# Kernel tuning notes

Hardware: AMD Instinct MI355X
Metric: run time of the kernel (lower is better)

The kernel has to match this reference:

```python
import jax, jax.numpy as jnp
import numpy as np

B, H, S, D, R = 2, 32, 1024, 128, 16
NB = 4  # max blocks: pre-image, image, pre-assistant-end, post-assistant


def _make_block_mask():
    # Synthetic but realistic block boundaries per sample (derived from the
    # image-token run and assistant-token subsequence positions that the torch
    # module extracts host-side from input_ids).
    bounds = [
        [(0, 16), (16, 272), (272, 603), (603, S)],
        [(0, 8), (8, 264), (264, 501), (501, S)],
    ]
    m = np.zeros((B, NB, S), np.float32)
    for b, blocks in enumerate(bounds):
        for n, (s, e) in enumerate(blocks):
            m[b, n, s:e] = 1.0
    return jnp.asarray(m)


def setup_inputs() -> dict:
    key = jax.random.key(0)
    ks = jax.random.split(key, 7)
    hid = H * D  # 4096
    lo = H * R   # 512
    causal_masked = ~jnp.tril(jnp.ones((S, S), bool))  # True = masked
    return {
        "query_states": jax.random.normal(ks[0], (B, H, S, D), jnp.float32),
        "key_states": jax.random.normal(ks[1], (B, H, S, D), jnp.float32),
        "Wqa": jax.random.normal(ks[2], (lo, hid), jnp.float32) / np.sqrt(hid),
        "Wqb": jax.random.normal(ks[3], (hid, lo), jnp.float32) / np.sqrt(lo),
        "Wka": jax.random.normal(ks[4], (lo, hid), jnp.float32) / np.sqrt(hid),
        "Wkb": jax.random.normal(ks[5], (hid, lo), jnp.float32) / np.sqrt(lo),
        "alpha": jax.random.normal(ks[6], (1,), jnp.float32) * 0.01,  # alpha_std
        "block_mask": _make_block_mask(),  # [B, NB, K] 1.0 inside block
        "attention_mask": jnp.broadcast_to(causal_masked, (B, 1, S, S)),
    }


def reference(query_states, key_states, Wqa, Wqb, Wka, Wkb, alpha, block_mask, attention_mask):
    Bb, Hh, Q, Dd = query_states.shape
    scaling = Dd ** -0.5

    # low-rank Q projection: [B,H,Q,D] -> [B,Q,H*D] -> rank -> back
    q = query_states.transpose(0, 2, 1, 3).reshape(Bb, Q, Hh * Dd)
    q = (q @ Wqa.T) @ Wqb.T
    q = q.reshape(Bb, Q, Hh, Dd).transpose(0, 2, 1, 3)

    Kk = key_states.shape[2]
    k = key_states.transpose(0, 2, 1, 3).reshape(Bb, Kk, Hh * Dd)
    k = (k @ Wka.T) @ Wkb.T
    k = k.reshape(Bb, Kk, Hh, Dd).transpose(0, 2, 1, 3)

    scores = jnp.einsum('bhqd,bhkd->bhqk', q, k) * scaling  # [B,H,Q,K]
    neg = jnp.finfo(scores.dtype).min
    scores = jnp.where(attention_mask, neg, scores)
    attn = jax.nn.softmax(scores, axis=-1)

    # block-wise mean pooling with causal-valid counts (mean_pool path)
    valid = (~attention_mask[:, 0]).astype(attn.dtype)       # [B,Q,K]
    masked_attn = attn * valid[:, None]                      # zero masked keys
    counts = jnp.einsum('bqk,bnk->bqn', valid, block_mask)   # [B,Q,NB]
    sums = jnp.einsum('bhqk,bnk->bhqn', masked_attn, block_mask)
    block_scores = sums / jnp.maximum(counts, 1.0)[:, None]  # [B,H,Q,NB]

    # expand block scores back to full [B,H,Q,K] and zero masked positions
    reweight = jnp.einsum('bhqn,bnk->bhqk', block_scores, block_mask)
    reweight = reweight * valid[:, None]
    return alpha[0] * reweight
```

## Files before the change

kernel.cpp:

```cpp
#include <hip/hip_runtime.h>
#include <hip/hip_bf16.h>

typedef float  f32x4 __attribute__((ext_vector_type(4)));
typedef _Float16 f16x8 __attribute__((ext_vector_type(8)));

#define S_LEN 1024
#define NHEAD 32
#define DHEAD 128
#define HID   4096
#define LORA  512
#define MROWS 2048

__global__ __launch_bounds__(256) void proj1_kernel(
    const float* __restrict__ Xq, const float* __restrict__ Wq_,
    const float* __restrict__ Xk, const float* __restrict__ Wk_,
    _Float16* __restrict__ Uq, _Float16* __restrict__ Uk)
{
  const float* X = blockIdx.z ? Xk : Xq;
  const float* W = blockIdx.z ? Wk_ : Wq_;
  _Float16*    U = blockIdx.z ? Uk  : Uq;

  __shared__ _Float16 As[128 * 40];
  __shared__ _Float16 Bs[64 * 40];

  const int t = threadIdx.x;
  const int lane = t & 63, w = t >> 6;
  const int wr = w >> 1, wc = w & 1;
  const int m0 = blockIdx.x * 128, n0 = blockIdx.y * 64;

  const int ar = t >> 1, ac = (t & 1) * 16;
  const int am = m0 + ar, ab = am >> 10, as_ = am & 1023;
  const float* Abase = X + (size_t)ab * (NHEAD * S_LEN * DHEAD) + (size_t)as_ * DHEAD;
  const int br = t >> 2, bc = (t & 3) * 8;
  const float* Brow = W + (size_t)(n0 + br) * HID;

  f32x4 acc[4][2] = {};

  for (int kt = 0; kt < HID / 32; ++kt) {
    const int kg = kt * 32 + ac;
    const float* pa = Abase + (size_t)(kg >> 7) * (S_LEN * DHEAD) + (kg & 127);
    f32x4 v0 = *(const f32x4*)(pa + 0);
    f32x4 v1 = *(const f32x4*)(pa + 4);
    f32x4 v2 = *(const f32x4*)(pa + 8);
    f32x4 v3 = *(const f32x4*)(pa + 12);
    f16x8 h0, h1;
#pragma unroll
    for (int i = 0; i < 4; ++i) {
      h0[i] = (_Float16)v0[i]; h0[i + 4] = (_Float16)v1[i];
      h1[i] = (_Float16)v2[i]; h1[i + 4] = (_Float16)v3[i];
    }
    const float* pb = Brow + kt * 32 + bc;
    f32x4 u0 = *(const f32x4*)(pb + 0);
    f32x4 u1 = *(const f32x4*)(pb + 4);
    f16x8 hb;
#pragma unroll
    for (int i = 0; i < 4; ++i) { hb[i] = (_Float16)u0[i]; hb[i + 4] = (_Float16)u1[i]; }

    __syncthreads();
    *(f16x8*)&As[ar * 40 + ac]     = h0;
    *(f16x8*)&As[ar * 40 + ac + 8] = h1;
    *(f16x8*)&Bs[br * 40 + bc]     = hb;
    __syncthreads();

    f16x8 afr[4], bfr[2];
#pragma unroll
    for (int im = 0; im < 4; ++im)
      afr[im] = *(const f16x8*)&As[(wr * 64 + im * 16 + (lane & 15)) * 40 + (lane >> 4) * 8];
#pragma unroll
    for (int in = 0; in < 2; ++in)
      bfr[in] = *(const f16x8*)&Bs[(wc * 32 + in * 16 + (lane & 15)) * 40 + (lane >> 4) * 8];
#pragma unroll
    for (int im = 0; im < 4; ++im)
#pragma unroll
      for (int in = 0; in < 2; ++in)
        acc[im][in] = __builtin_amdgcn_mfma_f32_16x16x32_f16(afr[im], bfr[in], acc[im][in], 0, 0, 0);
  }

#pragma unroll
  for (int im = 0; im < 4; ++im)
#pragma unroll
    for (int in = 0; in < 2; ++in)
#pragma unroll
      for (int j = 0; j < 4; ++j) {
        const int m = m0 + wr * 64 + im * 16 + (lane >> 4) * 4 + j;
        const int n = n0 + wc * 32 + in * 16 + (lane & 15);
        U[(size_t)m * LORA + n] = (_Float16)acc[im][in][j];
      }
}

__global__ __launch_bounds__(256) void proj2_kernel(
    const _Float16* __restrict__ Uq, const float* __restrict__ Wq_,
    const _Float16* __restrict__ Uk, const float* __restrict__ Wk_,
    _Float16* __restrict__ Pq, _Float16* __restrict__ Pk)
{
  const _Float16* U = blockIdx.z ? Uk : Uq;
  const float*    W = blockIdx.z ? Wk_ : Wq_;
  _Float16*       P = blockIdx.z ? Pk : Pq;

  __shared__ _Float16 As[128 * 40];
  __shared__ _Float16 Bs[64 * 40];

  const int t = threadIdx.x;
  const int lane = t & 63, w = t >> 6;
  const int wr = w >> 1, wc = w & 1;
  const int m0 = blockIdx.x * 128, n0 = blockIdx.y * 64;

  const int ar = t >> 1, ac = (t & 1) * 16;
  const _Float16* Arow = U + (size_t)(m0 + ar) * LORA;
  const int br = t >> 2, bc = (t & 3) * 8;
  const float* Brow = W + (size_t)(n0 + br) * LORA;

  f32x4 acc[4][2] = {};

  for (int kt = 0; kt < LORA / 32; ++kt) {
    const _Float16* pa = Arow + kt * 32 + ac;
    f16x8 h0 = *(const f16x8*)(pa + 0);
    f16x8 h1 = *(const f16x8*)(pa + 8);
    const float* pb = Brow + kt * 32 + bc;
    f32x4 u0 = *(const f32x4*)(pb + 0);
    f32x4 u1 = *(const f32x4*)(pb + 4);
    f16x8 hb;
#pragma unroll
    for (int i = 0; i < 4; ++i) { hb[i] = (_Float16)u0[i]; hb[i + 4] = (_Float16)u1[i]; }

    __syncthreads();
    *(f16x8*)&As[ar * 40 + ac]     = h0;
    *(f16x8*)&As[ar * 40 + ac + 8] = h1;
    *(f16x8*)&Bs[br * 40 + bc]     = hb;
    __syncthreads();

    f16x8 afr[4], bfr[2];
#pragma unroll
    for (int im = 0; im < 4; ++im)
      afr[im] = *(const f16x8*)&As[(wr * 64 + im * 16 + (lane & 15)) * 40 + (lane >> 4) * 8];
#pragma unroll
    for (int in = 0; in < 2; ++in)
      bfr[in] = *(const f16x8*)&Bs[(wc * 32 + in * 16 + (lane & 15)) * 40 + (lane >> 4) * 8];
#pragma unroll
    for (int im = 0; im < 4; ++im)
#pragma unroll
      for (int in = 0; in < 2; ++in)
        acc[im][in] = __builtin_amdgcn_mfma_f32_16x16x32_f16(afr[im], bfr[in], acc[im][in], 0, 0, 0);
  }

#pragma unroll
  for (int im = 0; im < 4; ++im)
#pragma unroll
    for (int in = 0; in < 2; ++in)
#pragma unroll
      for (int j = 0; j < 4; ++j) {
        const int m = m0 + wr * 64 + im * 16 + (lane >> 4) * 4 + j;
        const int n = n0 + wc * 32 + in * 16 + (lane & 15);
        P[(size_t)m * HID + n] = (_Float16)acc[im][in][j];
      }
}

__global__ __launch_bounds__(256) void attn_kernel(
    const _Float16* __restrict__ QP, const _Float16* __restrict__ KP,
    const float* __restrict__ bmask, const float* __restrict__ alphap,
    float* __restrict__ out)
{
  __shared__ float    bm[1024 * 4];
  __shared__ _Float16 kv[64 * 136];
  __shared__ float    bs_l[64 * 4];

  const int t = threadIdx.x;
  const int lane = t & 63, w = t >> 6;
  const int bh = blockIdx.x, b = bh >> 5, h = bh & 31;
  const int qb = (int)(gridDim.y - 1) - (int)blockIdx.y;

  for (int idx = t; idx < 4096; idx += 256) {
    const int nb = idx >> 10, k = idx & 1023;
    bm[k * 4 + nb] = bmask[(size_t)b * 4096 + idx];
  }

  const int qrow = qb * 64 + w * 16 + (lane & 15);
  const _Float16* qrp = QP + (size_t)(b * 1024 + qrow) * HID + h * DHEAD;
  f16x8 a[4];
#pragma unroll
  for (int i = 0; i < 4; ++i)
    a[i] = *(const f16x8*)(qrp + i * 32 + (lane >> 4) * 8);

  float L[4] = {0.f, 0.f, 0.f, 0.f};
  float bsum[4][4] = {};
  float cnt[4][4] = {};
  const float scale = 0.08838834764831845f;

  const int r = t >> 2, c = (t & 3) * 32;
  const _Float16* kbase = KP + (size_t)(b * 1024) * HID + h * DHEAD;

  for (int kt = 0; kt <= qb; ++kt) {
    const _Float16* pk = kbase + (size_t)(kt * 64 + r) * HID + c;
    f16x8 k0 = *(const f16x8*)(pk + 0);
    f16x8 k1 = *(const f16x8*)(pk + 8);
    f16x8 k2 = *(const f16x8*)(pk + 16);
    f16x8 k3 = *(const f16x8*)(pk + 24);
    __syncthreads();
    *(f16x8*)&kv[r * 136 + c + 0]  = k0;
    *(f16x8*)&kv[r * 136 + c + 8]  = k1;
    *(f16x8*)&kv[r * 136 + c + 16] = k2;
    *(f16x8*)&kv[r * 136 + c + 24] = k3;
    __syncthreads();

#pragma unroll
    for (int nt = 0; nt < 4; ++nt) {
      f32x4 sacc = {0.f, 0.f, 0.f, 0.f};
#pragma unroll
      for (int i = 0; i < 4; ++i) {
        f16x8 bf = *(const f16x8*)&kv[(nt * 16 + (lane & 15)) * 136 + i * 32 + (lane >> 4) * 8];
        sacc = __builtin_amdgcn_mfma_f32_16x16x32_f16(a[i], bf, sacc, 0, 0, 0);
      }
      const int kk = kt * 64 + nt * 16 + (lane & 15);
      f32x4 mv = *(const f32x4*)&bm[kk * 4];
#pragma unroll
      for (int j = 0; j < 4; ++j) {
        const int q = qb * 64 + w * 16 + (lane >> 4) * 4 + j;
        const bool valid = (kk <= q);
        const float e = valid ? __expf(sacc[j] * scale) : 0.f;
        const float vf = valid ? 1.f : 0.f;
        L[j] += e;
        bsum[0][j] += e * mv[0];  cnt[0][j] += vf * mv[0];
        bsum[1][j] += e * mv[1];  cnt[1][j] += vf * mv[1];
        bsum[2][j] += e * mv[2];  cnt[2][j] += vf * mv[2];
        bsum[3][j] += e * mv[3];  cnt[3][j] += vf * mv[3];
      }
    }
  }

#pragma unroll
  for (int j = 0; j < 4; ++j) {
#pragma unroll
    for (int m = 1; m < 16; m <<= 1) {
      L[j] += __shfl_xor(L[j], m, 64);
#pragma unroll
      for (int nb = 0; nb < 4; ++nb) {
        bsum[nb][j] += __shfl_xor(bsum[nb][j], m, 64);
        cnt[nb][j]  += __shfl_xor(cnt[nb][j], m, 64);
      }
    }
  }
  if ((lane & 15) == 0) {
#pragma unroll
    for (int j = 0; j < 4; ++j) {
      const int rr = w * 16 + (lane >> 4) * 4 + j;
      const float invL = 1.f / L[j];
#pragma unroll
      for (int nb = 0; nb < 4; ++nb)
        bs_l[rr * 4 + nb] = bsum[nb][j] * invL / fmaxf(cnt[nb][j], 1.f);
    }
  }
  __syncthreads();

  const float alpha = alphap[0];
  const size_t obase = ((size_t)bh * 1024 + (size_t)qb * 64) * 1024;
  for (int rr = 0; rr < 64; ++rr) {
    const int q = qb * 64 + rr;
    f32x4 bsv = *(const f32x4*)&bs_l[rr * 4];
    const int k0 = t * 4;
    f32x4 m0v = *(const f32x4*)&bm[(k0 + 0) * 4];
    f32x4 m1v = *(const f32x4*)&bm[(k0 + 1) * 4];
    f32x4 m2v = *(const f32x4*)&bm[(k0 + 2) * 4];
    f32x4 m3v = *(const f32x4*)&bm[(k0 + 3) * 4];
    f32x4 o;
    o[0] = (k0 + 0 <= q) ? alpha * (bsv[0]*m0v[0] + bsv[1]*m0v[1] + bsv[2]*m0v[2] + bsv[3]*m0v[3]) : 0.f;
    o[1] = (k0 + 1 <= q) ? alpha * (bsv[0]*m1v[0] + bsv[1]*m1v[1] + bsv[2]*m1v[2] + bsv[3]*m1v[3]) : 0.f;
    o[2] = (k0 + 2 <= q) ? alpha * (bsv[0]*m2v[0] + bsv[1]*m2v[1] + bsv[2]*m2v[2] + bsv[3]*m2v[3]) : 0.f;
    o[3] = (k0 + 3 <= q) ? alpha * (bsv[0]*m3v[0] + bsv[1]*m3v[1] + bsv[2]*m3v[2] + bsv[3]*m3v[3]) : 0.f;
    *(f32x4*)(out + obase + (size_t)rr * 1024 + k0) = o;
  }
}

extern "C" void kernel_launch(void* const* d_in, const int* in_sizes, int n_in,
                              void* d_out, int out_size, void* d_ws, size_t ws_size,
                              hipStream_t stream) {
  const float* q     = (const float*)d_in[0];
  const float* k     = (const float*)d_in[1];
  const float* Wqa   = (const float*)d_in[2];
  const float* Wqb   = (const float*)d_in[3];
  const float* Wka   = (const float*)d_in[4];
  const float* Wkb   = (const float*)d_in[5];
  const float* alpha = (const float*)d_in[6];
  const float* bmask = (const float*)d_in[7];
  float* out = (float*)d_out;

  _Float16* Uq = (_Float16*)d_ws;
  _Float16* Uk = Uq + (size_t)MROWS * LORA;
  _Float16* Pq = Uk + (size_t)MROWS * LORA;
  _Float16* Pk = Pq + (size_t)MROWS * HID;

  proj1_kernel<<<dim3(16, 8, 2),  256, 0, stream>>>(q, Wqa, k, Wka, Uq, Uk);
  proj2_kernel<<<dim3(16, 64, 2), 256, 0, stream>>>(Uq, Wqb, Uk, Wkb, Pq, Pk);
  attn_kernel <<<dim3(64, 16),    256, 0, stream>>>(Pq, Pk, bmask, alpha, out);
}
```

Measured before the change: 538.4 us.

## Pre-convert inputs to fp16, use LDS-direct GEMM, simplify attention block sums

Adds a conversion kernel that casts activations (into token-major layout) and weights to fp16 up front. The two projections are replaced by one shared GEMM that loads tiles straight into LDS with global_load_lds on 128x128 tiles, dropping the per-tile conversion in the main loop. The attention kernel now takes causal counts from a prefix sum of the block mask, gets the softmax denominator from the block sums, and skips fully masked MFMA tiles on the diagonal. This adds a full extra pass over memory for conversion and leaves only 128 blocks for the first GEMM. The LDS tiles are unpadded, so bank conflicts may increase.

```diff
diff --git a/kernel.cpp b/kernel.cpp
--- a/kernel.cpp
+++ b/kernel.cpp
@@ -1,8 +1,9 @@
 #include <hip/hip_runtime.h>
 #include <hip/hip_bf16.h>
 
-typedef float  f32x4 __attribute__((ext_vector_type(4)));
+typedef float    f32x4 __attribute__((ext_vector_type(4)));
 typedef _Float16 f16x8 __attribute__((ext_vector_type(8)));
+typedef unsigned int u32;
 
 #define S_LEN 1024
 #define NHEAD 32
@@ -11,147 +12,113 @@
 #define LORA  512
 #define MROWS 2048
 
-__global__ __launch_bounds__(256) void proj1_kernel(
-    const float* __restrict__ Xq, const float* __restrict__ Wq_,
-    const float* __restrict__ Xk, const float* __restrict__ Wk_,
-    _Float16* __restrict__ Uq, _Float16* __restrict__ Uk)
+__device__ __forceinline__ void gload16(const void* g, const void* l) {
+  __builtin_amdgcn_global_load_lds(
+      (const __attribute__((address_space(1))) u32*)g,
+      (__attribute__((address_space(3))) u32*)l, 16, 0, 0);
+}
+
+#define XCH  1048576
+#define WCH  262144
+#define TOTCH (2*XCH + 4*WCH)
+
+__global__ __launch_bounds__(256) void convert_kernel(
+    const float* __restrict__ Xq, const float* __restrict__ Xk,
+    const float* __restrict__ Wqa, const float* __restrict__ Wka,
+    const float* __restrict__ Wqb, const float* __restrict__ Wkb,
+    _Float16* __restrict__ XqH, _Float16* __restrict__ XkH,
+    _Float16* __restrict__ WaqH, _Float16* __restrict__ WakH,
+    _Float16* __restrict__ WbqH, _Float16* __restrict__ WbkH)
 {
-  const float* X = blockIdx.z ? Xk : Xq;
-  const float* W = blockIdx.z ? Wk_ : Wq_;
-  _Float16*    U = blockIdx.z ? Uk  : Uq;
-
-  __shared__ _Float16 As[128 * 40];
-  __shared__ _Float16 Bs[64 * 40];
-
-  const int t = threadIdx.x;
-  const int lane = t & 63, w = t >> 6;
+  for (int c = blockIdx.x * 256 + threadIdx.x; c < TOTCH; c += 2048 * 256) {
+    const float* src;
+    _Float16* dst;
+    if (c < 2 * XCH) {
+      const int cc = (c < XCH) ? c : c - XCH;
+      const float* X = (c < XCH) ? Xq : Xk;
+      _Float16*  XH = (c < XCH) ? XqH : XkH;
+      const int row = cc >> 9;
+      const int col8 = cc & 511;
+      const int h = col8 >> 4, d0 = (col8 & 15) * 8;
+      const int b = row >> 10, s = row & 1023;
+      src = X + (((size_t)(b * NHEAD + h)) * S_LEN + s) * DHEAD + d0;
+      dst = XH + (size_t)row * HID + col8 * 8;
+    } else {
+      const int cw = c - 2 * XCH;
+      const int seg = cw / WCH;
+      const int off = (cw - seg * WCH) * 8;
+      const float* Ws[4] = {Wqa, Wka, Wqb, Wkb};
+      _Float16*  Wd[4] = {WaqH, WakH, WbqH, WbkH};
+      src = Ws[seg] + off;
+      dst = Wd[seg] + off;
+    }
+    f32x4 v0 = *(const f32x4*)(src + 0);
+    f32x4 v1 = *(const f32x4*)(src + 4);
+    f16x8 h8;
+#pragma unroll
+    for (int i = 0; i < 4; ++i) { h8[i] = (_Float16)v0[i]; h8[i + 4] = (_Float16)v1[i]; }
+    *(f16x8*)dst = h8;
+  }
+}
+
+__global__ __launch_bounds__(256) void gemm_f16(
+    const _Float16* __restrict__ Aq, const _Float16* __restrict__ Bq,
+    _Float16* __restrict__ Cq,
+    const _Float16* __restrict__ Ak, const _Float16* __restrict__ Bk,
+    _Float16* __restrict__ Ck, int K, int N)
+{
+  const _Float16* A = blockIdx.z ? Ak : Aq;
+  const _Float16* B = blockIdx.z ? Bk : Bq;
+  _Float16*       C = blockIdx.z ? Ck : Cq;
+
+  __shared__ _Float16 As[128 * 32];
+  __shared__ _Float16 Bs[128 * 32];
+
+  const int t = threadIdx.x, lane = t & 63, w = t >> 6;
   const int wr = w >> 1, wc = w & 1;
-  const int m0 = blockIdx.x * 128, n0 = blockIdx.y * 64;
-
-  const int ar = t >> 1, ac = (t & 1) * 16;
-  const int am = m0 + ar, ab = am >> 10, as_ = am & 1023;
-  const float* Abase = X + (size_t)ab * (NHEAD * S_LEN * DHEAD) + (size_t)as_ * DHEAD;
-  const int br = t >> 2, bc = (t & 3) * 8;
-  const float* Brow = W + (size_t)(n0 + br) * HID;
-
-  f32x4 acc[4][2] = {};
-
-  for (int kt = 0; kt < HID / 32; ++kt) {
-    const int kg = kt * 32 + ac;
-    const float* pa = Abase + (size_t)(kg >> 7) * (S_LEN * DHEAD) + (kg & 127);
-    f32x4 v0 = *(const f32x4*)(pa + 0);
-    f32x4 v1 = *(const f32x4*)(pa + 4);
-    f32x4 v2 = *(const f32x4*)(pa + 8);
-    f32x4 v3 = *(const f32x4*)(pa + 12);
-    f16x8 h0, h1;
-#pragma unroll
-    for (int i = 0; i < 4; ++i) {
-      h0[i] = (_Float16)v0[i]; h0[i + 4] = (_Float16)v1[i];
-      h1[i] = (_Float16)v2[i]; h1[i + 4] = (_Float16)v3[i];
-    }
-    const float* pb = Brow + kt * 32 + bc;
-    f32x4 u0 = *(const f32x4*)(pb + 0);
-    f32x4 u1 = *(const f32x4*)(pb + 4);
-    f16x8 hb;
-#pragma unroll
-    for (int i = 0; i < 4; ++i) { hb[i] = (_Float16)u0[i]; hb[i + 4] = (_Float16)u1[i]; }
-
-    __syncthreads();
-    *(f16x8*)&As[ar * 40 + ac]     = h0;
-    *(f16x8*)&As[ar * 40 + ac + 8] = h1;
-    *(f16x8*)&Bs[br * 40 + bc]     = hb;
-    __syncthreads();
-
-    f16x8 afr[4], bfr[2];
+  const int m0 = blockIdx.x * 128, n0 = blockIdx.y * 128;
+
+  const int o0 = w * 1024 + lane * 16;
+  const int o1 = o0 + 4096;
+  const int r0 = o0 >> 6, k0e = (o0 & 63) >> 1;
+  const int r1 = o1 >> 6, k1e = (o1 & 63) >> 1;
+
+  char* AsB = (char*)As;
+  char* BsB = (char*)Bs;
+
+  f32x4 acc[4][4] = {};
+
+  for (int kt = 0; kt < K; kt += 32) {
+    __syncthreads();
+    gload16(A + (size_t)(m0 + r0) * K + kt + k0e, AsB + w * 1024);
+    gload16(A + (size_t)(m0 + r1) * K + kt + k1e, AsB + 4096 + w * 1024);
+    gload16(B + (size_t)(n0 + r0) * K + kt + k0e, BsB + w * 1024);
+    gload16(B + (size_t)(n0 + r1) * K + kt + k1e, BsB + 4096 + w * 1024);
+    __syncthreads();
+
+    f16x8 af[4], bf[4];
 #pragma unroll
     for (int im = 0; im < 4; ++im)
-      afr[im] = *(const f16x8*)&As[(wr * 64 + im * 16 + (lane & 15)) * 40 + (lane >> 4) * 8];
-#pragma unroll
-    for (int in = 0; in < 2; ++in)
-      bfr[in] = *(const f16x8*)&Bs[(wc * 32 + in * 16 + (lane & 15)) * 40 + (lane >> 4) * 8];
+      af[im] = *(const f16x8*)(AsB + (wr * 64 + im * 16 + (lane & 15)) * 64 + (lane >> 4) * 16);
+#pragma unroll
+    for (int in = 0; in < 4; ++in)
+      bf[in] = *(const f16x8*)(BsB + (wc * 64 + in * 16 + (lane & 15)) * 64 + (lane >> 4) * 16);
 #pragma unroll
     for (int im = 0; im < 4; ++im)
 #pragma unroll
-      for (int in = 0; in < 2; ++in)
-        acc[im][in] = __builtin_amdgcn_mfma_f32_16x16x32_f16(afr[im], bfr[in], acc[im][in], 0, 0, 0);
+      for (int in = 0; in < 4; ++in)
+        acc[im][in] = __builtin_amdgcn_mfma_f32_16x16x32_f16(af[im], bf[in], acc[im][in], 0, 0, 0);
   }
 
 #pragma unroll
   for (int im = 0; im < 4; ++im)
 #pragma unroll
-    for (int in = 0; in < 2; ++in)
+    for (int in = 0; in < 4; ++in)
 #pragma unroll
       for (int j = 0; j < 4; ++j) {
         const int m = m0 + wr * 64 + im * 16 + (lane >> 4) * 4 + j;
-        const int n = n0 + wc * 32 + in * 16 + (lane & 15);
-        U[(size_t)m * LORA + n] = (_Float16)acc[im][in][j];
-      }
-}
-
-__global__ __launch_bounds__(256) void proj2_kernel(
-    const _Float16* __restrict__ Uq, const float* __restrict__ Wq_,
-    const _Float16* __restrict__ Uk, const float* __restrict__ Wk_,
-    _Float16* __restrict__ Pq, _Float16* __restrict__ Pk)
-{
-  const _Float16* U = blockIdx.z ? Uk : Uq;
-  const float*    W = blockIdx.z ? Wk_ : Wq_;
-  _Float16*       P = blockIdx.z ? Pk : Pq;
-
-  __shared__ _Float16 As[128 * 40];
-  __shared__ _Float16 Bs[64 * 40];
-
-  const int t = threadIdx.x;
-  const int lane = t & 63, w = t >> 6;
-  const int wr = w >> 1, wc = w & 1;
-  const int m0 = blockIdx.x * 128, n0 = blockIdx.y * 64;
-
-  const int ar = t >> 1, ac = (t & 1) * 16;
-  const _Float16* Arow = U + (size_t)(m0 + ar) * LORA;
-  const int br = t >> 2, bc = (t & 3) * 8;
-  const float* Brow = W + (size_t)(n0 + br) * LORA;
-
-  f32x4 acc[4][2] = {};
-
-  for (int kt = 0; kt < LORA / 32; ++kt) {
-    const _Float16* pa = Arow + kt * 32 + ac;
-    f16x8 h0 = *(const f16x8*)(pa + 0);
-    f16x8 h1 = *(const f16x8*)(pa + 8);
-    const float* pb = Brow + kt * 32 + bc;
-    f32x4 u0 = *(const f32x4*)(pb + 0);
-    f32x4 u1 = *(const f32x4*)(pb + 4);
-    f16x8 hb;
-#pragma unroll
-    for (int i = 0; i < 4; ++i) { hb[i] = (_Float16)u0[i]; hb[i + 4] = (_Float16)u1[i]; }
-
-    __syncthreads();
-    *(f16x8*)&As[ar * 40 + ac]     = h0;
-    *(f16x8*)&As[ar * 40 + ac + 8] = h1;
-    *(f16x8*)&Bs[br * 40 + bc]     = hb;
-    __syncthreads();
-
-    f16x8 afr[4], bfr[2];
-#pragma unroll
-    for (int im = 0; im < 4; ++im)
-      afr[im] = *(const f16x8*)&As[(wr * 64 + im * 16 + (lane & 15)) * 40 + (lane >> 4) * 8];
-#pragma unroll
-    for (int in = 0; in < 2; ++in)
-      bfr[in] = *(const f16x8*)&Bs[(wc * 32 + in * 16 + (lane & 15)) * 40 + (lane >> 4) * 8];
-#pragma unroll
-    for (int im = 0; im < 4; ++im)
-#pragma unroll
-      for (int in = 0; in < 2; ++in)
-        acc[im][in] = __builtin_amdgcn_mfma_f32_16x16x32_f16(afr[im], bfr[in], acc[im][in], 0, 0, 0);
-  }
-
-#pragma unroll
-  for (int im = 0; im < 4; ++im)
-#pragma unroll
-    for (int in = 0; in < 2; ++in)
-#pragma unroll
-      for (int j = 0; j < 4; ++j) {
-        const int m = m0 + wr * 64 + im * 16 + (lane >> 4) * 4 + j;
-        const int n = n0 + wc * 32 + in * 16 + (lane & 15);
-        P[(size_t)m * HID + n] = (_Float16)acc[im][in][j];
+        const int n = n0 + wc * 64 + in * 16 + (lane & 15);
+        C[(size_t)m * N + n] = (_Float16)acc[im][in][j];
       }
 }
 
@@ -161,6 +128,7 @@
     float* __restrict__ out)
 {
   __shared__ float    bm[1024 * 4];
+  __shared__ float    pf[1024 * 4];
   __shared__ _Float16 kv[64 * 136];
   __shared__ float    bs_l[64 * 4];
 
@@ -173,6 +141,21 @@
     const int nb = idx >> 10, k = idx & 1023;
     bm[k * 4 + nb] = bmask[(size_t)b * 4096 + idx];
   }
+  __syncthreads();
+
+  {
+    float carry = 0.f;
+    for (int seg = 0; seg < 16; ++seg) {
+      float v = bm[(seg * 64 + lane) * 4 + w];
+#pragma unroll
+      for (int d = 1; d < 64; d <<= 1) {
+        float u = __shfl_up(v, d, 64);
+        if (lane >= d) v += u;
+      }
+      pf[(seg * 64 + lane) * 4 + w] = v + carry;
+      carry += __shfl(v, 63, 64);
+    }
+  }
 
   const int qrow = qb * 64 + w * 16 + (lane & 15);
   const _Float16* qrp = QP + (size_t)(b * 1024 + qrow) * HID + h * DHEAD;
@@ -181,9 +164,7 @@
   for (int i = 0; i < 4; ++i)
     a[i] = *(const f16x8*)(qrp + i * 32 + (lane >> 4) * 8);
 
-  float L[4] = {0.f, 0.f, 0.f, 0.f};
   float bsum[4][4] = {};
-  float cnt[4][4] = {};
   const float scale = 0.08838834764831845f;
 
   const int r = t >> 2, c = (t & 3) * 32;
@@ -202,8 +183,10 @@
     *(f16x8*)&kv[r * 136 + c + 24] = k3;
     __syncthreads();
 
+    const bool last = (kt == qb);
 #pragma unroll
     for (int nt = 0; nt < 4; ++nt) {
+      if (last && nt > w) break;
       f32x4 sacc = {0.f, 0.f, 0.f, 0.f};
 #pragma unroll
       for (int i = 0; i < 4; ++i) {
@@ -212,41 +195,40 @@
       }
       const int kk = kt * 64 + nt * 16 + (lane & 15);
       f32x4 mv = *(const f32x4*)&bm[kk * 4];
+      const bool diag = last && (nt == w);
 #pragma unroll
       for (int j = 0; j < 4; ++j) {
-        const int q = qb * 64 + w * 16 + (lane >> 4) * 4 + j;
-        const bool valid = (kk <= q);
-        const float e = valid ? __expf(sacc[j] * scale) : 0.f;
-        const float vf = valid ? 1.f : 0.f;
-        L[j] += e;
-        bsum[0][j] += e * mv[0];  cnt[0][j] += vf * mv[0];
-        bsum[1][j] += e * mv[1];  cnt[1][j] += vf * mv[1];
-        bsum[2][j] += e * mv[2];  cnt[2][j] += vf * mv[2];
-        bsum[3][j] += e * mv[3];  cnt[3][j] += vf * mv[3];
-      }
-    }
-  }
-
-#pragma unroll
-  for (int j = 0; j < 4; ++j) {
-#pragma unroll
-    for (int m = 1; m < 16; m <<= 1) {
-      L[j] += __shfl_xor(L[j], m, 64);
-#pragma unroll
-      for (int nb = 0; nb < 4; ++nb) {
+        float e = __expf(sacc[j] * scale);
+        if (diag) {
+          const int q = qb * 64 + w * 16 + (lane >> 4) * 4 + j;
+          e = (kk <= q) ? e : 0.f;
+        }
+        bsum[0][j] += e * mv[0];
+        bsum[1][j] += e * mv[1];
+        bsum[2][j] += e * mv[2];
+        bsum[3][j] += e * mv[3];
+      }
+    }
+  }
+
+#pragma unroll
+  for (int j = 0; j < 4; ++j)
+#pragma unroll
+    for (int m = 1; m < 16; m <<= 1)
+#pragma unroll
+      for (int nb = 0; nb < 4; ++nb)
         bsum[nb][j] += __shfl_xor(bsum[nb][j], m, 64);
-        cnt[nb][j]  += __shfl_xor(cnt[nb][j], m, 64);
-      }
-    }
-  }
+
   if ((lane & 15) == 0) {
 #pragma unroll
     for (int j = 0; j < 4; ++j) {
       const int rr = w * 16 + (lane >> 4) * 4 + j;
-      const float invL = 1.f / L[j];
+      const int q = qb * 64 + rr;
+      const float Lr = bsum[0][j] + bsum[1][j] + bsum[2][j] + bsum[3][j];
+      const float invL = 1.f / Lr;
 #pragma unroll
       for (int nb = 0; nb < 4; ++nb)
-        bs_l[rr * 4 + nb] = bsum[nb][j] * invL / fmaxf(cnt[nb][j], 1.f);
+        bs_l[rr * 4 + nb] = bsum[nb][j] * invL / fmaxf(pf[q * 4 + nb], 1.f);
     }
   }
   __syncthreads();
@@ -283,12 +265,20 @@
   const float* bmask = (const float*)d_in[7];
   float* out = (float*)d_out;
 
-  _Float16* Uq = (_Float16*)d_ws;
-  _Float16* Uk = Uq + (size_t)MROWS * LORA;
-  _Float16* Pq = Uk + (size_t)MROWS * LORA;
-  _Float16* Pk = Pq + (size_t)MROWS * HID;
-
-  proj1_kernel<<<dim3(16, 8, 2),  256, 0, stream>>>(q, Wqa, k, Wka, Uq, Uk);
-  proj2_kernel<<<dim3(16, 64, 2), 256, 0, stream>>>(Uq, Wqb, Uk, Wkb, Pq, Pk);
-  attn_kernel <<<dim3(64, 16),    256, 0, stream>>>(Pq, Pk, bmask, alpha, out);
-}
+  _Float16* XqH  = (_Float16*)d_ws;
+  _Float16* XkH  = XqH  + (size_t)MROWS * HID;
+  _Float16* WaqH = XkH  + (size_t)MROWS * HID;
+  _Float16* WakH = WaqH + (size_t)LORA * HID;
+  _Float16* WbqH = WakH + (size_t)LORA * HID;
+  _Float16* WbkH = WbqH + (size_t)HID * LORA;
+  _Float16* Uq   = WbkH + (size_t)HID * LORA;
+  _Float16* Uk   = Uq   + (size_t)MROWS * LORA;
+  _Float16* Pq   = Uk   + (size_t)MROWS * LORA;
+  _Float16* Pk   = Pq   + (size_t)MROWS * HID;
+
+  convert_kernel<<<2048, 256, 0, stream>>>(q, k, Wqa, Wka, Wqb, Wkb,
+                                           XqH, XkH, WaqH, WakH, WbqH, WbkH);
+  gemm_f16<<<dim3(16, 4, 2),  256, 0, stream>>>(XqH, WaqH, Uq, XkH, WakH, Uk, HID, LORA);
+  gemm_f16<<<dim3(16, 32, 2), 256, 0, stream>>>(Uq, WbqH, Pq, Uk, WbkH, Pk, LORA, HID);
+  attn_kernel<<<dim3(64, 16), 256, 0, stream>>>(Pq, Pk, bmask, alpha, out);
+}
```

New measurement: 507.2 us. 5.8% less time.
